# Kernel tuning notes

Hardware: AMD Instinct MI355X
Metric: run time of the kernel (lower is better)

## Reference

```python
import jax, jax.numpy as jnp
import numpy as np

BATCH = 2048
NUM_NODES = 512
HIDDEN = 64
LEVELS = 3
LN_EPS = 1e-5
NEG_SLOPE = 0.01


def setup_inputs() -> dict:
    key = jax.random.key(0)
    k1, k2, k3 = jax.random.split(key, 3)
    node_features = jax.random.normal(k1, (BATCH, NUM_NODES, HIDDEN), dtype=jnp.float32)
    # wavelet filters initialized exactly as _initialize_wavelet_filters
    h0 = jnp.array([0.683, 1.183, 0.317, -0.183], dtype=jnp.float32)
    h1 = jnp.array([-0.183, -0.317, 1.183, -0.683], dtype=jnp.float32)
    lvl_scale = 1.0 - 0.1 * jnp.arange(LEVELS, dtype=jnp.float32)  # [L]
    dec_filters = lvl_scale[:, None] * h0[None, :]  # [L, 4]
    rec_filters = lvl_scale[:, None] * h1[None, :]  # [L, 4]
    # per-node Linear(hidden, hidden): torch default init ~ U(-1/sqrt(H), 1/sqrt(H))
    bound = 1.0 / np.sqrt(HIDDEN)
    W = jax.random.uniform(k2, (NUM_NODES, HIDDEN, HIDDEN), minval=-bound, maxval=bound, dtype=jnp.float32)
    b = jax.random.uniform(k3, (NUM_NODES, HIDDEN), minval=-bound, maxval=bound, dtype=jnp.float32)
    gamma = jnp.ones((NUM_NODES, HIDDEN), dtype=jnp.float32)
    beta = jnp.zeros((NUM_NODES, HIDDEN), dtype=jnp.float32)
    # scale_map from the module; nodes not in the map default to level 0
    scale_map = {0: 0, 1: 1, 3: 2, 7: 2, 6: 1, 4: 0, 2: 1, 5: 1, 8: 0}
    scales_np = np.zeros(NUM_NODES, dtype=np.int32)
    for i, v in scale_map.items():
        scales_np[i] = v % LEVELS
    scales = jnp.asarray(scales_np)
    return {
        "node_features": node_features,
        "dec_filters": dec_filters,
        "rec_filters": rec_filters,
        "W": W,
        "b": b,
        "gamma": gamma,
        "beta": beta,
        "scales": scales,
    }


def reference(node_features, dec_filters, rec_filters, W, b, gamma, beta, scales):
    # The original pads a length-1 per-channel signal with (1,2) -> [0, x, 0, 0]
    # and cross-correlates with a size-4 filter, so the conv output is exactly
    # x * filter[1]. approx + detail == x * (h0[level,1] + h1[level,1]).
    s = dec_filters[scales, 1] + rec_filters[scales, 1]  # [N]
    wav = node_features * s[None, :, None]               # [B, N, H]
    # per-node Linear: y = x @ W_i^T + b_i, batched over nodes
    t = jnp.einsum("bnh,nkh->bnk", wav, W) + b[None]      # [B, N, H]
    # per-node LayerNorm over the hidden dim (torch eps=1e-5, biased var)
    mu = jnp.mean(t, axis=-1, keepdims=True)
    var = jnp.mean((t - mu) ** 2, axis=-1, keepdims=True)
    ln = (t - mu) / jnp.sqrt(var + LN_EPS) * gamma[None] + beta[None]
    # leaky_relu with negative_slope 0.01
    return jnp.where(ln >= 0, ln, NEG_SLOPE * ln)
```

## Files before the change

kernel.cpp:

```cpp
#include <hip/hip_runtime.h>
#include <hip/hip_bf16.h>

#define BATCH 2048
#define NNODES 512
#define HID 64
#define LN_EPS 1e-5f
#define NEG_SLOPE 0.01f

#define NPB 4
#define SUBS 8
#define RPW 128
#define TSTR 68

typedef __attribute__((ext_vector_type(8))) short bf16x8;
typedef __attribute__((ext_vector_type(4))) float f32x4;

__device__ __forceinline__ short f2bf(float f) {
    union { __hip_bfloat16 h; short s; } u;
    u.h = __float2bfloat16(f);
    return u.s;
}

#define WAITV4() asm volatile("s_waitcnt vmcnt(4)" ::: "memory")
#define WAITV8() asm volatile("s_waitcnt vmcnt(8)" ::: "memory")
#define WAITL0() asm volatile("s_waitcnt lgkmcnt(0)" ::: "memory")

__global__ __launch_bounds__(256, 3) void wv_mfma8_kernel(
    const float* __restrict__ x,
    const float* __restrict__ dec,
    const float* __restrict__ rec,
    const float* __restrict__ W,
    const float* __restrict__ bias,
    const float* __restrict__ gamma,
    const float* __restrict__ beta,
    const int*   __restrict__ scales,
    float* __restrict__ out)
{
    __shared__ float xStage[NPB][2][1024];
    __shared__ float tLds  [NPB][16][TSTR];
    __shared__ float muLds [NPB][16];
    __shared__ float rsLds [NPB][16];

    const int tid  = threadIdx.x;
    const int wave = tid >> 6;
    const int lane = tid & 63;
    const int l16  = lane & 15;
    const int lg   = lane >> 4;

    const int ng   = blockIdx.x & 127;
    const int rc   = blockIdx.x >> 7;
    const int node = ng * NPB + wave;
    const int b0   = rc * RPW;

    const int   sc   = scales[node];
    const float sfac = dec[sc * 4 + 1] + rec[sc * 4 + 1];

#define STAGE(sub_, buf_)                                                     \
    {                                                                         \
        const int s4_ = (lane & 15) * 4;                                      \
        const int rb_ = lane >> 4;                                            \
        _Pragma("unroll")                                                     \
        for (int k_ = 0; k_ < 4; ++k_) {                                      \
            const int r_ = k_ * 4 + rb_;                                      \
            const float* g_ = x + (size_t)(b0 + (sub_) * 16 + r_) *           \
                                  (NNODES * HID) + node * HID +               \
                                  (s4_ ^ ((r_ & 7) << 2));                    \
            __builtin_amdgcn_global_load_lds(                                 \
                (const __attribute__((address_space(1))) void*)g_,            \
                (__attribute__((address_space(3))) void*)                     \
                    (&xStage[wave][buf_][0] + k_ * 256),                      \
                16, 0, 0);                                                    \
        }                                                                     \
    }

    f32x4 wv[4][2][2];
    const float* Wn = W + (size_t)node * HID * HID;
    #pragma unroll
    for (int c = 0; c < 4; ++c) {
        #pragma unroll
        for (int s = 0; s < 2; ++s) {
            const float* p = Wn + (c * 16 + l16) * HID + s * 32 + lg * 8;
            wv[c][s][0] = *reinterpret_cast<const f32x4*>(p);
            wv[c][s][1] = *reinterpret_cast<const f32x4*>(p + 4);
        }
    }
    STAGE(0, 0);
    STAGE(1, 1);

    f32x4 bb[4];
    #pragma unroll
    for (int c = 0; c < 4; ++c)
        bb[c] = *reinterpret_cast<const f32x4*>(bias + node * HID + c * 16 + lg * 4);
    const f32x4 gg = *reinterpret_cast<const f32x4*>(gamma + node * HID + l16 * 4);
    const f32x4 be = *reinterpret_cast<const f32x4*>(beta  + node * HID + l16 * 4);

    bf16x8 wf[4][2];
    #pragma unroll
    for (int c = 0; c < 4; ++c) {
        #pragma unroll
        for (int s = 0; s < 2; ++s) {
            const f32x4 w0 = wv[c][s][0], w1 = wv[c][s][1];
            bf16x8 f;
            f[0] = f2bf(w0[0]); f[1] = f2bf(w0[1]); f[2] = f2bf(w0[2]); f[3] = f2bf(w0[3]);
            f[4] = f2bf(w1[0]); f[5] = f2bf(w1[1]); f[6] = f2bf(w1[2]); f[7] = f2bf(w1[3]);
            wf[c][s] = f;
        }
    }

    const int ro = l16 * 64;
    const int sw = (l16 & 7) << 2;

    #pragma unroll
    for (int sub = 0; sub < SUBS; ++sub) {
        if (sub == 0 || sub == SUBS - 1) { WAITV4(); } else { WAITV8(); }

        const float* Sb = &xStage[wave][sub & 1][0];
        const f32x4 x0 = *reinterpret_cast<const f32x4*>(Sb + ro + ((lg * 8     ) ^ sw));
        const f32x4 x1 = *reinterpret_cast<const f32x4*>(Sb + ro + ((lg * 8 + 4 ) ^ sw));
        const f32x4 x2 = *reinterpret_cast<const f32x4*>(Sb + ro + ((lg * 8 + 32) ^ sw));
        const f32x4 x3 = *reinterpret_cast<const f32x4*>(Sb + ro + ((lg * 8 + 36) ^ sw));

        bf16x8 af0, af1;
        af0[0] = f2bf(x0[0] * sfac); af0[1] = f2bf(x0[1] * sfac);
        af0[2] = f2bf(x0[2] * sfac); af0[3] = f2bf(x0[3] * sfac);
        af0[4] = f2bf(x1[0] * sfac); af0[5] = f2bf(x1[1] * sfac);
        af0[6] = f2bf(x1[2] * sfac); af0[7] = f2bf(x1[3] * sfac);
        af1[0] = f2bf(x2[0] * sfac); af1[1] = f2bf(x2[1] * sfac);
        af1[2] = f2bf(x2[2] * sfac); af1[3] = f2bf(x2[3] * sfac);
        af1[4] = f2bf(x3[0] * sfac); af1[5] = f2bf(x3[1] * sfac);
        af1[6] = f2bf(x3[2] * sfac); af1[7] = f2bf(x3[3] * sfac);

        f32x4 acc[4];
        #pragma unroll
        for (int c = 0; c < 4; ++c) {
            acc[c][0] = 0.f; acc[c][1] = 0.f; acc[c][2] = 0.f; acc[c][3] = 0.f;
            acc[c] = __builtin_amdgcn_mfma_f32_16x16x32_bf16(wf[c][0], af0, acc[c], 0, 0, 0);
            acc[c] = __builtin_amdgcn_mfma_f32_16x16x32_bf16(wf[c][1], af1, acc[c], 0, 0, 0);
        }

        float pS = 0.f;
        #pragma unroll
        for (int c = 0; c < 4; ++c) {
            #pragma unroll
            for (int i = 0; i < 4; ++i) {
                acc[c][i] += bb[c][i];
                pS += acc[c][i];
            }
        }
        pS += __shfl_xor(pS, 16, 64);
        pS += __shfl_xor(pS, 32, 64);
        const float mu = pS * (1.0f / 64.0f);

        float qS = 0.f;
        #pragma unroll
        for (int c = 0; c < 4; ++c) {
            #pragma unroll
            for (int i = 0; i < 4; ++i) {
                const float d = acc[c][i] - mu;
                qS += d * d;
            }
        }
        qS += __shfl_xor(qS, 16, 64);
        qS += __shfl_xor(qS, 32, 64);
        const float rstd = 1.0f / sqrtf(qS * (1.0f / 64.0f) + LN_EPS);

        #pragma unroll
        for (int c = 0; c < 4; ++c)
            *reinterpret_cast<f32x4*>(&tLds[wave][l16][c * 16 + lg * 4]) = acc[c];
        if (lg == 0) { muLds[wave][l16] = mu; rsLds[wave][l16] = rstd; }

        const int rowb = b0 + sub * 16;
        #pragma unroll
        for (int k = 0; k < 4; ++k) {
            const int rl = k * 4 + lg;
            f32x4 tv = *reinterpret_cast<const f32x4*>(&tLds[wave][rl][l16 * 4]);
            const float m  = muLds[wave][rl];
            const float rs = rsLds[wave][rl];
            f32x4 o;
            #pragma unroll
            for (int i = 0; i < 4; ++i) {
                float v = (tv[i] - m) * rs * gg[i] + be[i];
                o[i] = v >= 0.f ? v : v * NEG_SLOPE;
            }
            __builtin_nontemporal_store(
                o, reinterpret_cast<f32x4*>(
                       out + ((size_t)(rowb + rl) * NNODES + node) * HID + l16 * 4));
        }

        WAITL0();
        if (sub + 2 < SUBS) {
            STAGE(sub + 2, sub & 1);
        }
    }
#undef STAGE
}

extern "C" void kernel_launch(void* const* d_in, const int* in_sizes, int n_in,
                              void* d_out, int out_size, void* d_ws, size_t ws_size,
                              hipStream_t stream) {
    const float* x      = (const float*)d_in[0];
    const float* dec    = (const float*)d_in[1];
    const float* rec    = (const float*)d_in[2];
    const float* W      = (const float*)d_in[3];
    const float* bias   = (const float*)d_in[4];
    const float* gamma  = (const float*)d_in[5];
    const float* beta   = (const float*)d_in[6];
    const int*   scales = (const int*)d_in[7];
    float* out = (float*)d_out;

    const int blocks = (NNODES / NPB) * (BATCH / RPW);
    wv_mfma8_kernel<<<blocks, 256, 0, stream>>>(
        x, dec, rec, W, bias, gamma, beta, scales, out);
}
```

Measured before the change: 101.3 us.

## Reuse staging LDS for transpose, fold scale into weights, raise occupancy

Removes the separate tLds/muLds/rsLds shared arrays and writes the accumulator transpose into the just-consumed x staging buffer with the same XOR swizzle. Per-row mean and rstd now come from wave shuffles instead of LDS. The wavelet scale factor is folded into the bf16 weights once, which drops the per-element multiply on activations. Launch bounds go from 3 to 4 blocks per CU to use the smaller LDS footprint, which tightens the register budget. Reusing the staging buffer relies on the refill only being issued after the LDS reads finish.

```diff
diff --git a/kernel.cpp b/kernel.cpp
--- a/kernel.cpp
+++ b/kernel.cpp
@@ -10,7 +10,6 @@
 #define NPB 4
 #define SUBS 8
 #define RPW 128
-#define TSTR 68
 
 typedef __attribute__((ext_vector_type(8))) short bf16x8;
 typedef __attribute__((ext_vector_type(4))) float f32x4;
@@ -25,7 +24,7 @@
 #define WAITV8() asm volatile("s_waitcnt vmcnt(8)" ::: "memory")
 #define WAITL0() asm volatile("s_waitcnt lgkmcnt(0)" ::: "memory")
 
-__global__ __launch_bounds__(256, 3) void wv_mfma8_kernel(
+__global__ __launch_bounds__(256, 4) void wv_mfma9_kernel(
     const float* __restrict__ x,
     const float* __restrict__ dec,
     const float* __restrict__ rec,
@@ -37,9 +36,6 @@
     float* __restrict__ out)
 {
     __shared__ float xStage[NPB][2][1024];
-    __shared__ float tLds  [NPB][16][TSTR];
-    __shared__ float muLds [NPB][16];
-    __shared__ float rsLds [NPB][16];
 
     const int tid  = threadIdx.x;
     const int wave = tid >> 6;
@@ -101,8 +97,10 @@
         for (int s = 0; s < 2; ++s) {
             const f32x4 w0 = wv[c][s][0], w1 = wv[c][s][1];
             bf16x8 f;
-            f[0] = f2bf(w0[0]); f[1] = f2bf(w0[1]); f[2] = f2bf(w0[2]); f[3] = f2bf(w0[3]);
-            f[4] = f2bf(w1[0]); f[5] = f2bf(w1[1]); f[6] = f2bf(w1[2]); f[7] = f2bf(w1[3]);
+            f[0] = f2bf(w0[0] * sfac); f[1] = f2bf(w0[1] * sfac);
+            f[2] = f2bf(w0[2] * sfac); f[3] = f2bf(w0[3] * sfac);
+            f[4] = f2bf(w1[0] * sfac); f[5] = f2bf(w1[1] * sfac);
+            f[6] = f2bf(w1[2] * sfac); f[7] = f2bf(w1[3] * sfac);
             wf[c][s] = f;
         }
     }
@@ -114,21 +112,21 @@
     for (int sub = 0; sub < SUBS; ++sub) {
         if (sub == 0 || sub == SUBS - 1) { WAITV4(); } else { WAITV8(); }
 
-        const float* Sb = &xStage[wave][sub & 1][0];
+        float* Sb = &xStage[wave][sub & 1][0];
         const f32x4 x0 = *reinterpret_cast<const f32x4*>(Sb + ro + ((lg * 8     ) ^ sw));
         const f32x4 x1 = *reinterpret_cast<const f32x4*>(Sb + ro + ((lg * 8 + 4 ) ^ sw));
         const f32x4 x2 = *reinterpret_cast<const f32x4*>(Sb + ro + ((lg * 8 + 32) ^ sw));
         const f32x4 x3 = *reinterpret_cast<const f32x4*>(Sb + ro + ((lg * 8 + 36) ^ sw));
 
         bf16x8 af0, af1;
-        af0[0] = f2bf(x0[0] * sfac); af0[1] = f2bf(x0[1] * sfac);
-        af0[2] = f2bf(x0[2] * sfac); af0[3] = f2bf(x0[3] * sfac);
-        af0[4] = f2bf(x1[0] * sfac); af0[5] = f2bf(x1[1] * sfac);
-        af0[6] = f2bf(x1[2] * sfac); af0[7] = f2bf(x1[3] * sfac);
-        af1[0] = f2bf(x2[0] * sfac); af1[1] = f2bf(x2[1] * sfac);
-        af1[2] = f2bf(x2[2] * sfac); af1[3] = f2bf(x2[3] * sfac);
-        af1[4] = f2bf(x3[0] * sfac); af1[5] = f2bf(x3[1] * sfac);
-        af1[6] = f2bf(x3[2] * sfac); af1[7] = f2bf(x3[3] * sfac);
+        af0[0] = f2bf(x0[0]); af0[1] = f2bf(x0[1]);
+        af0[2] = f2bf(x0[2]); af0[3] = f2bf(x0[3]);
+        af0[4] = f2bf(x1[0]); af0[5] = f2bf(x1[1]);
+        af0[6] = f2bf(x1[2]); af0[7] = f2bf(x1[3]);
+        af1[0] = f2bf(x2[0]); af1[1] = f2bf(x2[1]);
+        af1[2] = f2bf(x2[2]); af1[3] = f2bf(x2[3]);
+        af1[4] = f2bf(x3[0]); af1[5] = f2bf(x3[1]);
+        af1[6] = f2bf(x3[2]); af1[7] = f2bf(x3[3]);
 
         f32x4 acc[4];
         #pragma unroll
@@ -166,16 +164,17 @@
 
         #pragma unroll
         for (int c = 0; c < 4; ++c)
-            *reinterpret_cast<f32x4*>(&tLds[wave][l16][c * 16 + lg * 4]) = acc[c];
-        if (lg == 0) { muLds[wave][l16] = mu; rsLds[wave][l16] = rstd; }
+            *reinterpret_cast<f32x4*>(
+                Sb + l16 * 64 + ((c * 16 + lg * 4) ^ ((l16 & 7) << 2))) = acc[c];
 
         const int rowb = b0 + sub * 16;
         #pragma unroll
         for (int k = 0; k < 4; ++k) {
             const int rl = k * 4 + lg;
-            f32x4 tv = *reinterpret_cast<const f32x4*>(&tLds[wave][rl][l16 * 4]);
-            const float m  = muLds[wave][rl];
-            const float rs = rsLds[wave][rl];
+            const f32x4 tv = *reinterpret_cast<const f32x4*>(
+                Sb + rl * 64 + ((l16 * 4) ^ ((rl & 7) << 2)));
+            const float m  = __shfl(mu,   rl, 64);
+            const float rs = __shfl(rstd, rl, 64);
             f32x4 o;
             #pragma unroll
             for (int i = 0; i < 4; ++i) {
@@ -209,6 +208,6 @@
     float* out = (float*)d_out;
 
     const int blocks = (NNODES / NPB) * (BATCH / RPW);
-    wv_mfma8_kernel<<<blocks, 256, 0, stream>>>(
+    wv_mfma9_kernel<<<blocks, 256, 0, stream>>>(
         x, dec, rec, W, bias, gamma, beta, scales, out);
 }
```

After: 136.9 us. +35.1%, slower.
